# Kernel optimization log

Hardware: AMD Instinct MI355X
Metric: run time of the kernel (lower is better)

Reference implementation:

```python
import jax, jax.numpy as jnp
import numpy as np

HID = 200
HALF = 100  # TreeLSTM hidden = hidden_size // 2
N_EDUS = 32768
N_STEPS = 2 * N_EDUS - 1


def setup_inputs() -> dict:
    key = jax.random.key(0)
    ks = jax.random.split(key, 16)
    s = 0.05  # keep logits / gates in a sane range
    d = {}
    d["enc_cls"] = jax.random.normal(ks[0], (N_EDUS, 768), jnp.float32)
    d["W_proj"] = jax.random.normal(ks[1], (HID, 768), jnp.float32) * s
    d["b_proj"] = jax.random.normal(ks[2], (HID,), jnp.float32) * s
    d["missing_node"] = jax.random.uniform(ks[3], (HID,), jnp.float32)
    d["W_act"] = jax.random.normal(ks[4], (2, 3 * HID), jnp.float32) * s
    d["b_act"] = jax.random.normal(ks[5], (2,), jnp.float32) * s
    d["W_lab"] = jax.random.normal(ks[6], (19, 3 * HID), jnp.float32) * s
    d["b_lab"] = jax.random.normal(ks[7], (19,), jnp.float32) * s
    d["W_dir"] = jax.random.normal(ks[8], (3, 3 * HID), jnp.float32) * s
    d["b_dir"] = jax.random.normal(ks[9], (3,), jnp.float32) * s
    d["W_tree"] = jax.random.normal(ks[10], (5 * HALF, 2 * HALF), jnp.float32) * s
    d["b_tree"] = jax.random.normal(ks[11], (5 * HALF,), jnp.float32) * s
    d["gold_action"] = jax.random.randint(ks[12], (N_STEPS,), 0, 2, jnp.int32)
    d["gold_label"] = jax.random.randint(ks[13], (N_STEPS,), 0, 19, jnp.int32)
    d["gold_direction"] = jax.random.randint(ks[14], (N_STEPS,), 0, 3, jnp.int32)
    return d


def reference(enc_cls, W_proj, b_proj, missing_node, W_act, b_act,
              W_lab, b_lab, W_dir, b_dir, W_tree, b_tree,
              gold_action, gold_label, gold_direction):
    N = enc_cls.shape[0]
    S = 2 * N - 1
    # BERT CLS -> project (dropout is identity in eval)
    enc = enc_cls @ W_proj.T + b_proj  # [N, 200]

    # deterministic left-branching gold schedule: shift, then (shift, reduce)*
    t = jnp.arange(S)
    is_shift = (t == 0) | (t % 2 == 1)

    def treelstm(e1, e2):
        # embeddings are concat(h, c), each HALF
        h1, c1 = e1[:HALF], e1[HALF:]
        h2, c2 = e2[:HALF], e2[HALF:]
        g = W_tree @ jnp.concatenate([h1, h2]) + b_tree  # [5*HALF]
        i, f1, f2, o, u = jnp.split(g, 5)
        c = jax.nn.sigmoid(i) * jnp.tanh(u) \
            + jax.nn.sigmoid(f1) * c1 + jax.nn.sigmoid(f2) * c2
        h = jax.nn.sigmoid(o) * jnp.tanh(c)
        return jnp.concatenate([h, c])

    def ce(logits, y):
        # CrossEntropyLoss for a single example
        return jax.nn.logsumexp(logits) - logits[y]

    def step(carry, xs):
        s1, s0, ptr = carry
        shift, ga, gl, gd = xs
        b = jnp.where(ptr < N, enc[jnp.minimum(ptr, N - 1)], missing_node)
        feats = jnp.concatenate([s1, s0, b])  # [600]
        loss = (ce(W_act @ feats + b_act, ga)
                + ce(W_lab @ feats + b_lab, gl)
                + ce(W_dir @ feats + b_dir, gd))
        merged = treelstm(s1, s0)
        s0n = jnp.where(shift, b, merged)
        s1n = jnp.where(shift, s0, missing_node)
        ptrn = ptr + shift.astype(ptr.dtype)
        return (s1n, s0n, ptrn), loss

    init = (missing_node, missing_node, jnp.int32(0))
    (_, root, _), losses = jax.lax.scan(
        step, init, (is_shift, gold_action, gold_label, gold_direction))
    return losses.sum()
```

## Files before the change

kernel.cpp:

```cpp
#include <hip/hip_runtime.h>
#include <cstdint>

#define HID 200
#define HALF 100
#define N_EDUS 32768
#define N_STEPS (2*N_EDUS - 1)
#define KMAX 32766
#define PSTRIDE 500

typedef __fp16 h2v __attribute__((ext_vector_type(2)));
typedef _Float16 f16x8 __attribute__((ext_vector_type(8)));
typedef float f32x4 __attribute__((ext_vector_type(4)));

__global__ __launch_bounds__(256) void gemm_bt(const float* __restrict__ A, int lda,
    const float* __restrict__ B, int ldb, const float* __restrict__ bias,
    float* __restrict__ C, int ldc, int M, int N, int K)
{
    __shared__ float As[32][68];
    __shared__ float Bs[32][68];
    const int tid = threadIdx.x;
    const int tx = tid & 15, ty = tid >> 4;
    const int m0 = blockIdx.x * 64, n0 = blockIdx.y * 64;
    float acc[4][4] = {};
    for (int kc = 0; kc < K; kc += 32) {
        const int kk = tid & 31, r0 = tid >> 5;
        #pragma unroll
        for (int p = 0; p < 8; ++p) {
            const int mm = r0 + p * 8;
            const int m = m0 + mm, n = n0 + mm, kg = kc + kk;
            As[kk][mm] = (m < M && kg < K) ? A[(size_t)m * lda + kg] : 0.f;
            Bs[kk][mm] = (n < N && kg < K) ? B[(size_t)n * ldb + kg] : 0.f;
        }
        __syncthreads();
        #pragma unroll
        for (int kk2 = 0; kk2 < 32; ++kk2) {
            const float4 a = *(const float4*)&As[kk2][tx * 4];
            const float4 b = *(const float4*)&Bs[kk2][ty * 4];
            const float av[4] = {a.x, a.y, a.z, a.w};
            const float bv[4] = {b.x, b.y, b.z, b.w};
            #pragma unroll
            for (int r = 0; r < 4; ++r)
                #pragma unroll
                for (int c = 0; c < 4; ++c)
                    acc[r][c] += av[r] * bv[c];
        }
        __syncthreads();
    }
    #pragma unroll
    for (int r = 0; r < 4; ++r) {
        const int m = m0 + tx * 4 + r;
        if (m >= M) continue;
        #pragma unroll
        for (int c = 0; c < 4; ++c) {
            const int n = n0 + ty * 4 + c;
            if (n < N) C[(size_t)m * ldc + n] = acc[r][c] + (bias ? bias[n] : 0.f);
        }
    }
}

__global__ void prep_kernel(const float* __restrict__ W_act, const float* __restrict__ W_lab,
    const float* __restrict__ W_dir, const float* __restrict__ miss,
    float* __restrict__ WAB, float* __restrict__ WBC,
    float* __restrict__ msAB, float* __restrict__ msBC, float* __restrict__ out)
{
    const int tid = threadIdx.x;
    if (tid == 0) out[0] = 0.f;
    for (int i = tid; i < 48 * 200; i += 256) {
        const int r = i / 200, c = i % 200;
        const int rr = r % 24;
        const float* src = (rr < 2) ? (W_act + rr * 600)
                         : (rr < 21) ? (W_lab + (rr - 2) * 600)
                                     : (W_dir + (rr - 21) * 600);
        WAB[i] = src[c + (r < 24 ? 0 : 200)];
        WBC[i] = src[c + (r < 24 ? 200 : 400)];
    }
    __syncthreads();
    if (tid < 48) {
        float sA = 0.f, sB = 0.f;
        for (int c = 0; c < 200; ++c) {
            sA += WAB[tid * 200 + c] * miss[c];
            sB += WBC[tid * 200 + c] * miss[c];
        }
        msAB[tid] = sA;
        msBC[tid] = sB;
    }
}

__global__ __launch_bounds__(256) void pack_wa(const float* __restrict__ W_tree,
                                               uint4* __restrict__ WA)
{
    const int i = blockIdx.x * 256 + threadIdx.x;
    if (i >= 8960) return;
    const int lane = i & 63, f = i >> 6;
    const int kc = f & 3, gw = f >> 2;
    const int w = gw % 7, g = gw / 7;
    const int row = w * 16 + (lane & 15);
    const int kb = kc * 32 + (lane >> 4) * 8;
    unsigned int dws[4];
    #pragma unroll
    for (int dw = 0; dw < 4; ++dw) {
        const int k0 = kb + dw * 2;
        float w0 = 0.f, w1 = 0.f;
        if (row < 100) {
            if (k0 < 100)     w0 = W_tree[(size_t)(g * 100 + row) * 200 + k0];
            if (k0 + 1 < 100) w1 = W_tree[(size_t)(g * 100 + row) * 200 + k0 + 1];
        }
        h2v h = __builtin_amdgcn_cvt_pkrtz(w0, w1);
        __builtin_memcpy(&dws[dw], &h, 4);
    }
    uint4 v; v.x = dws[0]; v.y = dws[1]; v.z = dws[2]; v.w = dws[3];
    WA[i] = v;
}

__device__ __forceinline__ float sigf(float x) {
    return __builtin_amdgcn_rcpf(1.f + __expf(-x));
}
__device__ __forceinline__ float tanhf_(float x) {
    return 1.f - 2.f * __builtin_amdgcn_rcpf(1.f + __expf(2.f * x));
}

#define BAR() asm volatile("s_waitcnt lgkmcnt(0)\n\ts_barrier" ::: "memory")

#define SELR(v) ((rsel & 2) ? ((rsel & 1) ? (v)[3] : (v)[2]) : ((rsel & 1) ? (v)[1] : (v)[0]))

#define BODY(U, DOLOAD) \
{ \
    const uint4* hb = (const uint4*)(&hbuf[(U) & 1][0]); \
    f16x8 bb[4]; \
    { \
        uint4 t0 = hb[kgrp];      uint4 t1 = hb[4 + kgrp]; \
        uint4 t2 = hb[8 + kgrp];  uint4 t3 = hb[12 + kgrp]; \
        __builtin_memcpy(&bb[0], &t0, 16); __builtin_memcpy(&bb[1], &t1, 16); \
        __builtin_memcpy(&bb[2], &t2, 16); __builtin_memcpy(&bb[3], &t3, 16); \
    } \
    f32x4 acc[5]; \
    _Pragma("unroll") \
    for (int g = 0; g < 5; ++g) acc[g] = (f32x4){0.f, 0.f, 0.f, 0.f}; \
    _Pragma("unroll") \
    for (int kc = 0; kc < 4; ++kc) { \
        _Pragma("unroll") \
        for (int g = 0; g < 5; ++g) \
            acc[g] = __builtin_amdgcn_mfma_f32_16x16x32_f16(A[g][kc], bb[kc], acc[g], 0, 0, 0); \
    } \
    const float gi  = SELR(acc[0]) + pr[U][0]; \
    const float gf1 = SELR(acc[1]) + pr[U][1]; \
    const float gf2 = SELR(acc[2]) + pr[U][2]; \
    const float go  = SELR(acc[3]) + pr[U][3]; \
    const float gu  = SELR(acc[4]) + pr[U][4]; \
    const float c2v = pr[U][5]; \
    if (DOLOAD) { \
        pr[U][0] = pP[0];   pr[U][1] = pP[100]; pr[U][2] = pP[200]; \
        pr[U][3] = pP[300]; pr[U][4] = pP[400]; pP += PSTRIDE; \
        pr[U][5] = *pE; pE += HID; \
    } \
    const float cnew = sigf(gi) * tanhf_(gu) + sigf(gf1) * c_sel + sigf(gf2) * c2v; \
    const float hnew = sigf(go) * tanhf_(cnew); \
    c_sel = cnew; \
    if (act) { \
        pM[0] = hnew; pM[100] = cnew; \
        hbuf[((U) & 1) ^ 1][row_c] = (_Float16)hnew; \
    } \
    pM += HID; \
    BAR(); \
}

__attribute__((amdgpu_flat_work_group_size(448, 448), amdgpu_waves_per_eu(2, 2)))
__global__ void chain_kernel(const float* __restrict__ enc,
    const uint4* __restrict__ WA, const float* __restrict__ P, float* __restrict__ M)
{
    const int T = threadIdx.x;
    const int wave = T >> 6, lane = T & 63;
    const int col = lane & 15, kgrp = lane >> 4;
    const int rsel = col & 3;
    const int row_c = wave * 16 + kgrp * 4 + rsel;
    const bool act = (col < 4) && (row_c < 100);
    __shared__ __align__(16) _Float16 hbuf[2][128];

    if (T < 200) M[T] = enc[T];
    if (T < 128) {
        hbuf[0][T] = (T < 100) ? (_Float16)enc[T] : (_Float16)0.f;
        hbuf[1][T] = (_Float16)0.f;
    }

    f16x8 A[5][4];
    #pragma unroll
    for (int g = 0; g < 5; ++g)
        #pragma unroll
        for (int kc = 0; kc < 4; ++kc) {
            uint4 t = WA[((g * 7 + wave) * 4 + kc) * 64 + lane];
            __builtin_memcpy(&A[g][kc], &t, 16);
        }

    float c_sel = enc[100 + row_c];

    float pr[4][6];
    #pragma unroll
    for (int u = 0; u < 4; ++u) {
        #pragma unroll
        for (int g = 0; g < 5; ++g)
            pr[u][g] = P[(size_t)(1 + u) * PSTRIDE + g * 100 + row_c];
        pr[u][5] = enc[(size_t)(1 + u) * HID + 100 + row_c];
    }
    const float* pP = P + (size_t)5 * PSTRIDE + row_c;
    const float* pE = enc + (size_t)5 * HID + 100 + row_c;
    float* pM = M + HID + row_c;
    BAR();

    for (int base = 1; base <= KMAX - 9; base += 4) {
        BODY(0, true);
        BODY(1, true);
        BODY(2, true);
        BODY(3, true);
    }
    BODY(0, true);
    BODY(1, true);
    BODY(2, false);
    BODY(3, false);
    BODY(0, false);
    BODY(1, false);
}

__global__ __launch_bounds__(256) void loss_kernel(const float* __restrict__ TM,
    const float* __restrict__ TE, const float* __restrict__ msAB, const float* __restrict__ msBC,
    const float* __restrict__ b_act, const float* __restrict__ b_lab, const float* __restrict__ b_dir,
    const int* __restrict__ ga, const int* __restrict__ gl, const int* __restrict__ gd,
    float* __restrict__ out)
{
    const int t = blockIdx.x * 256 + threadIdx.x;
    float loss = 0.f;
    if (t < N_STEPS) {
        const float *v1, *v0, *vb;
        if (t == 0)      { v1 = msAB; v0 = msAB + 24; vb = TE + 24; }
        else if (t == 1) { v1 = msAB; v0 = TE;        vb = TE + 48 + 24; }
        else if ((t & 1) == 0) {
            const int k = t >> 1;
            v1 = TM + (size_t)(k - 1) * 48;
            v0 = TE + (size_t)k * 48;
            vb = (k < N_EDUS - 1) ? (TE + (size_t)(k + 1) * 48 + 24) : (msBC + 24);
        } else {
            const int k = t >> 1;
            v1 = msAB;
            v0 = TM + (size_t)k * 48 + 24;
            vb = TE + (size_t)(k + 1) * 48 + 24;
        }
        float l[24];
        #pragma unroll
        for (int j = 0; j < 24; ++j) l[j] = v1[j] + v0[j] + vb[j];
        l[0] += b_act[0]; l[1] += b_act[1];
        #pragma unroll
        for (int j = 0; j < 19; ++j) l[2 + j] += b_lab[j];
        #pragma unroll
        for (int j = 0; j < 3; ++j) l[21 + j] += b_dir[j];
        const int ya = ga[t], yl = gl[t], yd = gd[t];
        {
            const float m = fmaxf(l[0], l[1]);
            const float sum = __expf(l[0] - m) + __expf(l[1] - m);
            loss += m + __logf(sum) - (ya == 0 ? l[0] : l[1]);
        }
        {
            float m = l[2];
            #pragma unroll
            for (int j = 1; j < 19; ++j) m = fmaxf(m, l[2 + j]);
            float sum = 0.f, ly = 0.f;
            #pragma unroll
            for (int j = 0; j < 19; ++j) {
                sum += __expf(l[2 + j] - m);
                if (j == yl) ly = l[2 + j];
            }
            loss += m + __logf(sum) - ly;
        }
        {
            const float m = fmaxf(fmaxf(l[21], l[22]), l[23]);
            const float sum = __expf(l[21] - m) + __expf(l[22] - m) + __expf(l[23] - m);
            const float ly = (yd == 0) ? l[21] : (yd == 1 ? l[22] : l[23]);
            loss += m + __logf(sum) - ly;
        }
    }
    #pragma unroll
    for (int off = 32; off > 0; off >>= 1) loss += __shfl_down(loss, off, 64);
    __shared__ float wsum[4];
    const int lane = threadIdx.x & 63, wv = threadIdx.x >> 6;
    if (lane == 0) wsum[wv] = loss;
    __syncthreads();
    if (threadIdx.x == 0) atomicAdd(out, wsum[0] + wsum[1] + wsum[2] + wsum[3]);
}

extern "C" void kernel_launch(void* const* d_in, const int* in_sizes, int n_in,
                              void* d_out, int out_size, void* d_ws, size_t ws_size,
                              hipStream_t stream) {
    const float* enc_cls = (const float*)d_in[0];
    const float* W_proj  = (const float*)d_in[1];
    const float* b_proj  = (const float*)d_in[2];
    const float* miss    = (const float*)d_in[3];
    const float* W_act   = (const float*)d_in[4];
    const float* b_act   = (const float*)d_in[5];
    const float* W_lab   = (const float*)d_in[6];
    const float* b_lab   = (const float*)d_in[7];
    const float* W_dir   = (const float*)d_in[8];
    const float* b_dir   = (const float*)d_in[9];
    const float* W_tree  = (const float*)d_in[10];
    const float* b_tree  = (const float*)d_in[11];
    const int*   ga      = (const int*)d_in[12];
    const int*   gl      = (const int*)d_in[13];
    const int*   gd      = (const int*)d_in[14];
    float* out = (float*)d_out;

    float* ws   = (float*)d_ws;
    float* enc  = ws;
    float* Mar  = ws + 6553600;
    float* P    = ws + 13107000;
    float* WAB  = ws + 29490500;
    float* WBC  = WAB + 9600;
    float* msAB = WBC + 9600;
    float* msBC = msAB + 48;
    uint4* WA   = (uint4*)(msBC + 48);
    float* TM = P;
    float* TE = P + 1572816;

    gemm_bt<<<dim3(512, 4, 1), 256, 0, stream>>>(enc_cls, 768, W_proj, 768, b_proj,
                                                 enc, 200, N_EDUS, 200, 768);
    gemm_bt<<<dim3(512, 8, 1), 256, 0, stream>>>(enc + 200, 200, W_tree + 100, 200, b_tree,
                                                 P + PSTRIDE, PSTRIDE, KMAX, 500, 100);
    prep_kernel<<<1, 256, 0, stream>>>(W_act, W_lab, W_dir, miss, WAB, WBC, msAB, msBC, out);
    pack_wa<<<35, 256, 0, stream>>>(W_tree, WA);
    chain_kernel<<<1, 448, 0, stream>>>(enc, WA, P, Mar);
    gemm_bt<<<dim3(512, 1, 1), 256, 0, stream>>>(Mar, 200, WAB, 200, nullptr,
                                                 TM, 48, KMAX + 1, 48, 200);
    gemm_bt<<<dim3(512, 1, 1), 256, 0, stream>>>(enc, 200, WBC, 200, nullptr,
                                                 TE, 48, N_EDUS, 48, 200);
    loss_kernel<<<dim3(256, 1, 1), 256, 0, stream>>>(TM, TE, msAB, msBC,
                                                     b_act, b_lab, b_dir, ga, gl, gd, out);
}
```

Baseline: 19.36 ms.

## Repack TreeLSTM gate rows densely across 8 waves and stage gates via LDS

```diff
diff --git a/kernel.cpp b/kernel.cpp
--- a/kernel.cpp
+++ b/kernel.cpp
@@ -90,20 +90,22 @@
                                                uint4* __restrict__ WA)
 {
     const int i = blockIdx.x * 256 + threadIdx.x;
-    if (i >= 8960) return;
+    if (i >= 8192) return;
     const int lane = i & 63, f = i >> 6;
-    const int kc = f & 3, gw = f >> 2;
-    const int w = gw % 7, g = gw / 7;
-    const int row = w * 16 + (lane & 15);
+    const int kc = f & 3, tw = f >> 2;
+    const int t = tw & 3, w = tw >> 2;
+    const int fr = w * 64 + t * 16 + (lane & 15);
     const int kb = kc * 32 + (lane >> 4) * 8;
     unsigned int dws[4];
     #pragma unroll
     for (int dw = 0; dw < 4; ++dw) {
         const int k0 = kb + dw * 2;
         float w0 = 0.f, w1 = 0.f;
-        if (row < 100) {
-            if (k0 < 100)     w0 = W_tree[(size_t)(g * 100 + row) * 200 + k0];
-            if (k0 + 1 < 100) w1 = W_tree[(size_t)(g * 100 + row) * 200 + k0 + 1];
+        if (fr < 500) {
+            const int g = fr / 100, rr = fr % 100;
+            const float* Wr = W_tree + (size_t)(g * 100 + rr) * 200;
+            if (k0 < 100)     w0 = Wr[k0];
+            if (k0 + 1 < 100) w1 = Wr[k0 + 1];
         }
         h2v h = __builtin_amdgcn_cvt_pkrtz(w0, w1);
         __builtin_memcpy(&dws[dw], &h, 4);
@@ -120,8 +122,7 @@
 }
 
 #define BAR() asm volatile("s_waitcnt lgkmcnt(0)\n\ts_barrier" ::: "memory")
-
-#define SELR(v) ((rsel & 2) ? ((rsel & 1) ? (v)[3] : (v)[2]) : ((rsel & 1) ? (v)[1] : (v)[0]))
+#define KEEP(x) asm volatile("" : "+v"(x))
 
 #define BODY(U, DOLOAD) \
 { \
@@ -133,48 +134,57 @@
         __builtin_memcpy(&bb[0], &t0, 16); __builtin_memcpy(&bb[1], &t1, 16); \
         __builtin_memcpy(&bb[2], &t2, 16); __builtin_memcpy(&bb[3], &t3, 16); \
     } \
-    f32x4 acc[5]; \
+    f32x4 acc[4]; \
     _Pragma("unroll") \
-    for (int g = 0; g < 5; ++g) acc[g] = (f32x4){0.f, 0.f, 0.f, 0.f}; \
-    _Pragma("unroll") \
-    for (int kc = 0; kc < 4; ++kc) { \
+    for (int t = 0; t < 4; ++t) { \
+        acc[t] = __builtin_amdgcn_mfma_f32_16x16x32_f16(A[t][0], bb[0], z4, 0, 0, 0); \
         _Pragma("unroll") \
-        for (int g = 0; g < 5; ++g) \
-            acc[g] = __builtin_amdgcn_mfma_f32_16x16x32_f16(A[g][kc], bb[kc], acc[g], 0, 0, 0); \
+        for (int kc = 1; kc < 4; ++kc) \
+            acc[t] = __builtin_amdgcn_mfma_f32_16x16x32_f16(A[t][kc], bb[kc], acc[t], 0, 0, 0); \
     } \
-    const float gi  = SELR(acc[0]) + pr[U][0]; \
-    const float gf1 = SELR(acc[1]) + pr[U][1]; \
-    const float gf2 = SELR(acc[2]) + pr[U][2]; \
-    const float go  = SELR(acc[3]) + pr[U][3]; \
-    const float gu  = SELR(acc[4]) + pr[U][4]; \
-    const float c2v = pr[U][5]; \
-    if (DOLOAD) { \
-        pr[U][0] = pP[0];   pr[U][1] = pP[100]; pr[U][2] = pP[200]; \
-        pr[U][3] = pP[300]; pr[U][4] = pP[400]; pP += PSTRIDE; \
-        pr[U][5] = *pE; pE += HID; \
+    if (col0) { \
+        _Pragma("unroll") \
+        for (int t = 0; t < 4; ++t) \
+            *(f32x4*)&G[gbase + t * 16] = acc[t]; \
     } \
-    const float cnew = sigf(gi) * tanhf_(gu) + sigf(gf1) * c_sel + sigf(gf2) * c2v; \
-    const float hnew = sigf(go) * tanhf_(cnew); \
-    c_sel = cnew; \
-    if (act) { \
-        pM[0] = hnew; pM[100] = cnew; \
-        hbuf[((U) & 1) ^ 1][row_c] = (_Float16)hnew; \
+    BAR(); \
+    if (wave < 2) { \
+        const float gi  = G[r]       + pr[U][0]; \
+        const float gf1 = G[100 + r] + pr[U][1]; \
+        const float gf2 = G[200 + r] + pr[U][2]; \
+        const float go  = G[300 + r] + pr[U][3]; \
+        const float gu  = G[400 + r] + pr[U][4]; \
+        const float c2v = pr[U][5]; \
+        if (DOLOAD) { \
+            pr[U][0] = pP[0];   pr[U][1] = pP[100]; pr[U][2] = pP[200]; \
+            pr[U][3] = pP[300]; pr[U][4] = pP[400]; pP += PSTRIDE; \
+            pr[U][5] = *pE; pE += HID; \
+        } \
+        const float cnew = sigf(gi) * tanhf_(gu) + sigf(gf1) * c_sel + sigf(gf2) * c2v; \
+        const float hnew = sigf(go) * tanhf_(cnew); \
+        c_sel = cnew; \
+        if (act) { \
+            pM[0] = hnew; pM[100] = cnew; \
+            hbuf[((U) & 1) ^ 1][r] = (_Float16)hnew; \
+        } \
+        pM += HID; \
     } \
-    pM += HID; \
     BAR(); \
 }
 
-__attribute__((amdgpu_flat_work_group_size(448, 448), amdgpu_waves_per_eu(2, 2)))
+__attribute__((amdgpu_flat_work_group_size(512, 512), amdgpu_waves_per_eu(2, 2)))
 __global__ void chain_kernel(const float* __restrict__ enc,
     const uint4* __restrict__ WA, const float* __restrict__ P, float* __restrict__ M)
 {
     const int T = threadIdx.x;
     const int wave = T >> 6, lane = T & 63;
-    const int col = lane & 15, kgrp = lane >> 4;
-    const int rsel = col & 3;
-    const int row_c = wave * 16 + kgrp * 4 + rsel;
-    const bool act = (col < 4) && (row_c < 100);
+    const int kgrp = lane >> 4;
+    const bool col0 = (lane & 15) == 0;
+    const int gbase = wave * 64 + kgrp * 4;
+    const int r = (wave << 6) | lane;
+    const bool act = (r < 100);
     __shared__ __align__(16) _Float16 hbuf[2][128];
+    __shared__ __align__(16) float G[640];
 
     if (T < 200) M[T] = enc[T];
     if (T < 128) {
@@ -182,28 +192,34 @@
         hbuf[1][T] = (_Float16)0.f;
     }
 
-    f16x8 A[5][4];
+    f16x8 A[4][4];
     #pragma unroll
-    for (int g = 0; g < 5; ++g)
+    for (int t = 0; t < 4; ++t)
         #pragma unroll
         for (int kc = 0; kc < 4; ++kc) {
-            uint4 t = WA[((g * 7 + wave) * 4 + kc) * 64 + lane];
-            __builtin_memcpy(&A[g][kc], &t, 16);
-        }
-
-    float c_sel = enc[100 + row_c];
-
+            uint4 tt = WA[(((wave * 4 + t) * 4) + kc) * 64 + lane];
+            __builtin_memcpy(&A[t][kc], &tt, 16);
+        }
+    f32x4 z4 = {0.f, 0.f, 0.f, 0.f};
+
+    float c_sel = 0.f;
     float pr[4][6];
-    #pragma unroll
-    for (int u = 0; u < 4; ++u) {
-        #pragma unroll
-        for (int g = 0; g < 5; ++g)
-            pr[u][g] = P[(size_t)(1 + u) * PSTRIDE + g * 100 + row_c];
-        pr[u][5] = enc[(size_t)(1 + u) * HID + 100 + row_c];
-    }
-    const float* pP = P + (size_t)5 * PSTRIDE + row_c;
-    const float* pE = enc + (size_t)5 * HID + 100 + row_c;
-    float* pM = M + HID + row_c;
+    const float* pP = P;
+    const float* pE = enc;
+    float* pM = M;
+    if (wave < 2) {
+        c_sel = enc[100 + r];
+        #pragma unroll
+        for (int u = 0; u < 4; ++u) {
+            #pragma unroll
+            for (int g = 0; g < 5; ++g)
+                pr[u][g] = P[(size_t)(1 + u) * PSTRIDE + g * 100 + r];
+            pr[u][5] = enc[(size_t)(1 + u) * HID + 100 + r];
+        }
+        pP = P + (size_t)5 * PSTRIDE + r;
+        pE = enc + (size_t)5 * HID + 100 + r;
+        pM = M + HID + r;
+    }
     BAR();
 
     for (int base = 1; base <= KMAX - 9; base += 4) {
@@ -322,8 +338,8 @@
     gemm_bt<<<dim3(512, 8, 1), 256, 0, stream>>>(enc + 200, 200, W_tree + 100, 200, b_tree,
                                                  P + PSTRIDE, PSTRIDE, KMAX, 500, 100);
     prep_kernel<<<1, 256, 0, stream>>>(W_act, W_lab, W_dir, miss, WAB, WBC, msAB, msBC, out);
-    pack_wa<<<35, 256, 0, stream>>>(W_tree, WA);
-    chain_kernel<<<1, 448, 0, stream>>>(enc, WA, P, Mar);
+    pack_wa<<<32, 256, 0, stream>>>(W_tree, WA);
+    chain_kernel<<<1, 512, 0, stream>>>(enc, WA, P, Mar);
     gemm_bt<<<dim3(512, 1, 1), 256, 0, stream>>>(Mar, 200, WAB, 200, nullptr,
                                                  TM, 48, KMAX + 1, 48, 200);
     gemm_bt<<<dim3(512, 1, 1), 256, 0, stream>>>(enc, 200, WBC, 200, nullptr,
```

Measured after the change: 24.42 ms. 1.26x slower.

## Swap MFMA operand roles and split K-accumulation into two independent chains

Applied to the files above, without the earlier changes.

```diff
diff --git a/kernel.cpp b/kernel.cpp
--- a/kernel.cpp
+++ b/kernel.cpp
@@ -86,14 +86,14 @@
     }
 }
 
-__global__ __launch_bounds__(256) void pack_wa(const float* __restrict__ W_tree,
-                                               uint4* __restrict__ WA)
+__global__ __launch_bounds__(256) void pack_wb(const float* __restrict__ W_tree,
+                                               uint4* __restrict__ WB)
 {
     const int i = blockIdx.x * 256 + threadIdx.x;
     if (i >= 8960) return;
     const int lane = i & 63, f = i >> 6;
     const int kc = f & 3, gw = f >> 2;
-    const int w = gw % 7, g = gw / 7;
+    const int g = gw % 5, w = gw / 5;
     const int row = w * 16 + (lane & 15);
     const int kb = kc * 32 + (lane >> 4) * 8;
     unsigned int dws[4];
@@ -102,14 +102,15 @@
         const int k0 = kb + dw * 2;
         float w0 = 0.f, w1 = 0.f;
         if (row < 100) {
-            if (k0 < 100)     w0 = W_tree[(size_t)(g * 100 + row) * 200 + k0];
-            if (k0 + 1 < 100) w1 = W_tree[(size_t)(g * 100 + row) * 200 + k0 + 1];
+            const float* Wr = W_tree + (size_t)(g * 100 + row) * 200;
+            if (k0 < 100)     w0 = Wr[k0];
+            if (k0 + 1 < 100) w1 = Wr[k0 + 1];
         }
         h2v h = __builtin_amdgcn_cvt_pkrtz(w0, w1);
         __builtin_memcpy(&dws[dw], &h, 4);
     }
     uint4 v; v.x = dws[0]; v.y = dws[1]; v.z = dws[2]; v.w = dws[3];
-    WA[i] = v;
+    WB[i] = v;
 }
 
 __device__ __forceinline__ float sigf(float x) {
@@ -120,8 +121,6 @@
 }
 
 #define BAR() asm volatile("s_waitcnt lgkmcnt(0)\n\ts_barrier" ::: "memory")
-
-#define SELR(v) ((rsel & 2) ? ((rsel & 1) ? (v)[3] : (v)[2]) : ((rsel & 1) ? (v)[1] : (v)[0]))
 
 #define BODY(U, DOLOAD) \
 { \
@@ -133,20 +132,24 @@
         __builtin_memcpy(&bb[0], &t0, 16); __builtin_memcpy(&bb[1], &t1, 16); \
         __builtin_memcpy(&bb[2], &t2, 16); __builtin_memcpy(&bb[3], &t3, 16); \
     } \
-    f32x4 acc[5]; \
+    f32x4 aA[5], aB[5]; \
     _Pragma("unroll") \
-    for (int g = 0; g < 5; ++g) acc[g] = (f32x4){0.f, 0.f, 0.f, 0.f}; \
+    for (int g = 0; g < 5; ++g) \
+        aA[g] = __builtin_amdgcn_mfma_f32_16x16x32_f16(bb[0], Wf[g][0], z4, 0, 0, 0); \
     _Pragma("unroll") \
-    for (int kc = 0; kc < 4; ++kc) { \
-        _Pragma("unroll") \
-        for (int g = 0; g < 5; ++g) \
-            acc[g] = __builtin_amdgcn_mfma_f32_16x16x32_f16(A[g][kc], bb[kc], acc[g], 0, 0, 0); \
-    } \
-    const float gi  = SELR(acc[0]) + pr[U][0]; \
-    const float gf1 = SELR(acc[1]) + pr[U][1]; \
-    const float gf2 = SELR(acc[2]) + pr[U][2]; \
-    const float go  = SELR(acc[3]) + pr[U][3]; \
-    const float gu  = SELR(acc[4]) + pr[U][4]; \
+    for (int g = 0; g < 5; ++g) \
+        aB[g] = __builtin_amdgcn_mfma_f32_16x16x32_f16(bb[2], Wf[g][2], z4, 0, 0, 0); \
+    _Pragma("unroll") \
+    for (int g = 0; g < 5; ++g) \
+        aA[g] = __builtin_amdgcn_mfma_f32_16x16x32_f16(bb[1], Wf[g][1], aA[g], 0, 0, 0); \
+    _Pragma("unroll") \
+    for (int g = 0; g < 5; ++g) \
+        aB[g] = __builtin_amdgcn_mfma_f32_16x16x32_f16(bb[3], Wf[g][3], aB[g], 0, 0, 0); \
+    const float gi  = aA[0][0] + aB[0][0] + pr[U][0]; \
+    const float gf1 = aA[1][0] + aB[1][0] + pr[U][1]; \
+    const float gf2 = aA[2][0] + aB[2][0] + pr[U][2]; \
+    const float go  = aA[3][0] + aB[3][0] + pr[U][3]; \
+    const float gu  = aA[4][0] + aB[4][0] + pr[U][4]; \
     const float c2v = pr[U][5]; \
     if (DOLOAD) { \
         pr[U][0] = pP[0];   pr[U][1] = pP[100]; pr[U][2] = pP[200]; \
@@ -158,7 +161,7 @@
     c_sel = cnew; \
     if (act) { \
         pM[0] = hnew; pM[100] = cnew; \
-        hbuf[((U) & 1) ^ 1][row_c] = (_Float16)hnew; \
+        hbuf[((U) & 1) ^ 1][r] = (_Float16)hnew; \
     } \
     pM += HID; \
     BAR(); \
@@ -166,14 +169,14 @@
 
 __attribute__((amdgpu_flat_work_group_size(448, 448), amdgpu_waves_per_eu(2, 2)))
 __global__ void chain_kernel(const float* __restrict__ enc,
-    const uint4* __restrict__ WA, const float* __restrict__ P, float* __restrict__ M)
+    const uint4* __restrict__ WB, const float* __restrict__ P, float* __restrict__ M)
 {
     const int T = threadIdx.x;
     const int wave = T >> 6, lane = T & 63;
     const int col = lane & 15, kgrp = lane >> 4;
-    const int rsel = col & 3;
-    const int row_c = wave * 16 + kgrp * 4 + rsel;
-    const bool act = (col < 4) && (row_c < 100);
+    const int r = wave * 16 + col;
+    const int rc = (r < 100) ? r : 99;
+    const bool act = (kgrp == 0) && (r < 100);
     __shared__ __align__(16) _Float16 hbuf[2][128];
 
     if (T < 200) M[T] = enc[T];
@@ -182,28 +185,29 @@
         hbuf[1][T] = (_Float16)0.f;
     }
 
-    f16x8 A[5][4];
+    f16x8 Wf[5][4];
     #pragma unroll
     for (int g = 0; g < 5; ++g)
         #pragma unroll
         for (int kc = 0; kc < 4; ++kc) {
-            uint4 t = WA[((g * 7 + wave) * 4 + kc) * 64 + lane];
-            __builtin_memcpy(&A[g][kc], &t, 16);
-        }
-
-    float c_sel = enc[100 + row_c];
+            uint4 tt = WB[(((wave * 5 + g) * 4) + kc) * 64 + lane];
+            __builtin_memcpy(&Wf[g][kc], &tt, 16);
+        }
+    f32x4 z4 = {0.f, 0.f, 0.f, 0.f};
+
+    float c_sel = enc[100 + rc];
 
     float pr[4][6];
     #pragma unroll
     for (int u = 0; u < 4; ++u) {
         #pragma unroll
         for (int g = 0; g < 5; ++g)
-            pr[u][g] = P[(size_t)(1 + u) * PSTRIDE + g * 100 + row_c];
-        pr[u][5] = enc[(size_t)(1 + u) * HID + 100 + row_c];
-    }
-    const float* pP = P + (size_t)5 * PSTRIDE + row_c;
-    const float* pE = enc + (size_t)5 * HID + 100 + row_c;
-    float* pM = M + HID + row_c;
+            pr[u][g] = P[(size_t)(1 + u) * PSTRIDE + g * 100 + rc];
+        pr[u][5] = enc[(size_t)(1 + u) * HID + 100 + rc];
+    }
+    const float* pP = P + (size_t)5 * PSTRIDE + rc;
+    const float* pE = enc + (size_t)5 * HID + 100 + rc;
+    float* pM = M + HID + r;
     BAR();
 
     for (int base = 1; base <= KMAX - 9; base += 4) {
@@ -313,7 +317,7 @@
     float* WBC  = WAB + 9600;
     float* msAB = WBC + 9600;
     float* msBC = msAB + 48;
-    uint4* WA   = (uint4*)(msBC + 48);
+    uint4* WB   = (uint4*)(msBC + 48);
     float* TM = P;
     float* TE = P + 1572816;
 
@@ -322,8 +326,8 @@
     gemm_bt<<<dim3(512, 8, 1), 256, 0, stream>>>(enc + 200, 200, W_tree + 100, 200, b_tree,
                                                  P + PSTRIDE, PSTRIDE, KMAX, 500, 100);
     prep_kernel<<<1, 256, 0, stream>>>(W_act, W_lab, W_dir, miss, WAB, WBC, msAB, msBC, out);
-    pack_wa<<<35, 256, 0, stream>>>(W_tree, WA);
-    chain_kernel<<<1, 448, 0, stream>>>(enc, WA, P, Mar);
+    pack_wb<<<35, 256, 0, stream>>>(W_tree, WB);
+    chain_kernel<<<1, 448, 0, stream>>>(enc, WB, P, Mar);
     gemm_bt<<<dim3(512, 1, 1), 256, 0, stream>>>(Mar, 200, WAB, 200, nullptr,
                                                  TM, 48, KMAX + 1, 48, 200);
     gemm_bt<<<dim3(512, 1, 1), 256, 0, stream>>>(enc, 200, WBC, 200, nullptr,
```

New measurement: 19.33 ms. About the same (-0.2%).
